# Optimization experiments

Hardware: AMD Instinct MI355X
Metric: run time of the kernel (lower is better)

Reference implementation:

```python
import jax, jax.numpy as jnp
import numpy as np


def _ln(x, g, b, eps=1e-5):
    mu = jnp.mean(x, axis=-1, keepdims=True)
    var = jnp.mean((x - mu) ** 2, axis=-1, keepdims=True)
    return (x - mu) / jnp.sqrt(var + eps) * g + b


def _cell(x, h, c, Wih, Whh, bih, bhh):
    # torch LSTM gate order: i, f, g, o
    gates = x @ Wih.T + h @ Whh.T + bih + bhh
    i, f, g, o = jnp.split(gates, 4, axis=-1)
    c_new = jax.nn.sigmoid(f) * c + jax.nn.sigmoid(i) * jnp.tanh(g)
    h_new = jax.nn.sigmoid(o) * jnp.tanh(c_new)
    return h_new, c_new


def _forward(physical, target_seq, enc_W1, enc_b1, enc_ln1_g, enc_ln1_b, enc_W2, enc_b2,
             enc_ln2_g, enc_ln2_b, Wih0, Whh0, bih0, bhh0, Wih1, Whh1, bih1, bhh1,
             ln_g, ln_b, proj_W, proj_b, head_W1, head_b1, head_W2, head_b2, init_input):
    B, T = target_seq.shape
    Hd = proj_b.shape[0]
    # physical encoder -> initial hidden (dropout in eval mode)
    e = jax.nn.relu(_ln(physical @ enc_W1.T + enc_b1, enc_ln1_g, enc_ln1_b))
    h0 = jnp.tanh(_ln(e @ enc_W2.T + enc_b2, enc_ln2_g, enc_ln2_b))  # (B,H)
    h_init = jnp.broadcast_to(h0, (2, 2, B, Hd))  # (layer, direction, B, H)
    c_init = jnp.zeros((2, 2, B, Hd), dtype=h0.dtype)
    # teacher forcing ratio = 1.0 -> inputs are known ahead of time
    x0 = jnp.broadcast_to(init_input, (B, 1))
    xs = jnp.concatenate([x0[None], jnp.swapaxes(target_seq, 0, 1)[:-1, :, None]], axis=0)  # (T,B,1)

    def step(carry, inp):
        h, c, prev = carry
        x, t = inp
        h0f, c0f = _cell(x, h[0, 0], c[0, 0], Wih0[0], Whh0[0], bih0[0], bhh0[0])
        h0b, c0b = _cell(x, h[0, 1], c[0, 1], Wih0[1], Whh0[1], bih0[1], bhh0[1])
        o0 = jnp.concatenate([h0f, h0b], axis=-1)  # (B,2H)
        h1f, c1f = _cell(o0, h[1, 0], c[1, 0], Wih1[0], Whh1[0], bih1[0], bhh1[0])
        h1b, c1b = _cell(o0, h[1, 1], c[1, 1], Wih1[1], Whh1[1], bih1[1], bhh1[1])
        out = _ln(jnp.concatenate([h1f, h1b], axis=-1), ln_g, ln_b)  # (B,2H)
        proj = out @ proj_W.T + proj_b  # (B,H)
        pred = jax.nn.relu(proj @ head_W1.T + head_b1) @ head_W2.T + head_b2  # (B,1)
        pred = jnp.where(t > 0, 0.8 * pred + 0.2 * prev, pred)
        h_new = jnp.stack([jnp.stack([h0f, h0b]), jnp.stack([h1f, h1b])])
        c_new = jnp.stack([jnp.stack([c0f, c0b]), jnp.stack([c1f, c1b])])
        return (h_new, c_new, pred), pred[:, 0]

    _, preds = jax.lax.scan(step, (h_init, c_init, jnp.zeros((B, 1), h0.dtype)),
                            (xs, jnp.arange(T)))
    return jnp.swapaxes(preds, 0, 1)  # (B,T)


def setup_inputs():
    B, P, Hd, T = 512, 16, 128, 128
    ks = iter(jax.random.split(jax.random.key(0), 40))
    rn = lambda shape, s=0.05: jax.random.normal(next(ks), shape, dtype=jnp.float32) * s
    return {
        "physical": jax.random.normal(next(ks), (B, P), dtype=jnp.float32),
        "target_seq": jax.random.normal(next(ks), (B, T), dtype=jnp.float32),
        "enc_W1": rn((2 * Hd, P)), "enc_b1": jnp.zeros((2 * Hd,), jnp.float32),
        "enc_ln1_g": jnp.ones((2 * Hd,), jnp.float32), "enc_ln1_b": jnp.zeros((2 * Hd,), jnp.float32),
        "enc_W2": rn((Hd, 2 * Hd)), "enc_b2": jnp.zeros((Hd,), jnp.float32),
        "enc_ln2_g": jnp.ones((Hd,), jnp.float32), "enc_ln2_b": jnp.zeros((Hd,), jnp.float32),
        "Wih0": rn((2, 4 * Hd, 1)), "Whh0": rn((2, 4 * Hd, Hd)),
        "bih0": jnp.zeros((2, 4 * Hd), jnp.float32), "bhh0": jnp.zeros((2, 4 * Hd), jnp.float32),
        "Wih1": rn((2, 4 * Hd, 2 * Hd)), "Whh1": rn((2, 4 * Hd, Hd)),
        "bih1": jnp.zeros((2, 4 * Hd), jnp.float32), "bhh1": jnp.zeros((2, 4 * Hd), jnp.float32),
        "ln_g": jnp.ones((2 * Hd,), jnp.float32), "ln_b": jnp.zeros((2 * Hd,), jnp.float32),
        "proj_W": rn((Hd, 2 * Hd)), "proj_b": jnp.zeros((Hd,), jnp.float32),
        "head_W1": rn((Hd, Hd)), "head_b1": jnp.zeros((Hd,), jnp.float32),
        "head_W2": rn((1, Hd)), "head_b2": jnp.zeros((1,), jnp.float32),
        "init_input": rn((1,), 0.02),
    }


def reference(physical, target_seq, enc_W1, enc_b1, enc_ln1_g, enc_ln1_b, enc_W2, enc_b2,
              enc_ln2_g, enc_ln2_b, Wih0, Whh0, bih0, bhh0, Wih1, Whh1, bih1, bhh1,
              ln_g, ln_b, proj_W, proj_b, head_W1, head_b1, head_W2, head_b2, init_input):
    return _forward(physical, target_seq, enc_W1, enc_b1, enc_ln1_g, enc_ln1_b, enc_W2, enc_b2,
                    enc_ln2_g, enc_ln2_b, Wih0, Whh0, bih0, bhh0, Wih1, Whh1, bih1, bhh1,
                    ln_g, ln_b, proj_W, proj_b, head_W1, head_b1, head_W2, head_b2, init_input)
```

## Files before the change

kernel.cpp:

```cpp
#include <hip/hip_runtime.h>
#include <hip/hip_bf16.h>

#define BB 512
#define TT 128

typedef unsigned short u16;
typedef short v8s __attribute__((ext_vector_type(8)));
typedef float f32x4 __attribute__((ext_vector_type(4)));

#define L2E  1.4426950408889634f
#define L2E2 2.8853900817779268f

__device__ __forceinline__ u16 f2bf(float x){
  union { float f; unsigned int u; } v; v.f = x;
  unsigned int r = (v.u + 0x7fffu + ((v.u >> 16) & 1u)) >> 16;
  return (u16)r;
}
__device__ __forceinline__ float bf2f(u16 u){
  union { unsigned int i; float f; } v; v.i = ((unsigned int)u) << 16; return v.f;
}
__device__ __forceinline__ float lo_bits(unsigned u){
  union { unsigned int i; float f; } v; v.i = u << 16; return v.f;
}
__device__ __forceinline__ float hi_bits(unsigned u){
  union { unsigned int i; float f; } v; v.i = u & 0xffff0000u; return v.f;
}
__device__ __forceinline__ uint2 pack4(f32x4 a){
  uint2 r;
  asm("v_cvt_pk_bf16_f32 %0, %1, %2" : "=v"(r.x) : "v"(a[0]), "v"(a[1]));
  asm("v_cvt_pk_bf16_f32 %0, %1, %2" : "=v"(r.y) : "v"(a[2]), "v"(a[3]));
  return r;
}
__device__ __forceinline__ float rcp_f(float x){ return __builtin_amdgcn_rcpf(x); }
#if defined(__has_builtin)
#if __has_builtin(__builtin_amdgcn_exp2f)
#define EXP2(x) __builtin_amdgcn_exp2f(x)
#endif
#endif
#ifndef EXP2
__device__ __forceinline__ float __exp2_asm(float x){
  float r; asm("v_exp_f32 %0, %1" : "=v"(r) : "v"(x)); return r;
}
#define EXP2(x) __exp2_asm(x)
#endif
__device__ __forceinline__ float sigm2(float y){ return rcp_f(1.f + EXP2(-y)); }
__device__ __forceinline__ float tanh2(float y){ return fmaf(2.f, sigm2(y), -1.f); }

__device__ __forceinline__ float tanh_f(float x){
  float e = __expf(-2.f * fabsf(x));
  float r = (1.f - e) * rcp_f(1.f + e);
  return copysignf(r, x);
}
__device__ __forceinline__ void bar_lds(){
  __builtin_amdgcn_sched_barrier(0);
  asm volatile("s_waitcnt lgkmcnt(0)" ::: "memory");
  __builtin_amdgcn_s_barrier();
  __builtin_amdgcn_sched_barrier(0);
}

__global__ __launch_bounds__(256) void k_prep(
    const float* tseq, const float* init_in,
    const float* Wih0, const float* Whh0, const float* bih0, const float* bhh0,
    const float* Wih1, const float* Whh1, const float* bih1, const float* bhh1,
    const float* projW, const float* hW1,
    float* xs, u16* W0p, u16* W1ip, u16* W1hp, u16* projWp, u16* hW1p,
    float* bias0, float* bias1, float* wv0)
{
  int tid = blockIdx.x * blockDim.x + threadIdx.x;
  int stride = gridDim.x * blockDim.x;
  for (int i = tid; i < TT*BB; i += stride){
    int t = i / BB, b = i % BB;
    xs[i] = (t == 0) ? init_in[0] : tseq[b*TT + (t-1)];
  }
  for (int i = tid; i < 2*512*128; i += stride){
    int d = i / (512*128), r = i % (512*128);
    int j = r / 128, k = r % 128;
    float sc = ((j >> 7) == 2) ? L2E2 : L2E;
    int dst = ((((d*32 + (j>>4))*4 + (k>>5))*64) + ((j&15) + 16*((k&31)>>3)))*8 + (k&7);
    W0p[dst]  = f2bf(Whh0[i] * sc);
    W1hp[dst] = f2bf(Whh1[i] * sc);
  }
  for (int i = tid; i < 2*512*256; i += stride){
    int d = i / (512*256), r = i % (512*256);
    int j = r / 256, k = r % 256;
    float sc = ((j >> 7) == 2) ? L2E2 : L2E;
    int dst = ((((d*32 + (j>>4))*8 + (k>>5))*64) + ((j&15) + 16*((k&31)>>3)))*8 + (k&7);
    W1ip[dst] = f2bf(Wih1[i] * sc);
  }
  for (int i = tid; i < 128*256; i += stride){
    int j = i / 256, k = i % 256;
    int dst = ((((j>>4)*8 + (k>>5))*64) + ((j&15) + 16*((k&31)>>3)))*8 + (k&7);
    projWp[dst] = f2bf(projW[i]);
  }
  for (int i = tid; i < 128*128; i += stride){
    int j = i / 128, k = i % 128;
    int dst = ((((j>>4)*4 + (k>>5))*64) + ((j&15) + 16*((k&31)>>3)))*8 + (k&7);
    hW1p[dst] = f2bf(hW1[i]);
  }
  for (int i = tid; i < 2*512; i += stride){
    float sc = (((i & 511) >> 7) == 2) ? L2E2 : L2E;
    bias0[i] = (bih0[i] + bhh0[i]) * sc;
    bias1[i] = (bih1[i] + bhh1[i]) * sc;
    wv0[i]   = Wih0[i] * sc;
  }
}

__global__ __launch_bounds__(256) void k_enc(
    const float* phys, const float* W1, const float* b1, const float* g1, const float* be1,
    const float* W2, const float* b2, const float* g2, const float* be2, float* h0enc)
{
  __shared__ float eL[8][256];
  int tid = threadIdx.x;
  int rr = tid >> 5, sub = tid & 31;
  int r = blockIdx.x * 8 + rr;
  float x[16];
#pragma unroll
  for (int k = 0; k < 16; ++k) x[k] = phys[r*16 + k];
  float y[8];
#pragma unroll
  for (int jj = 0; jj < 8; ++jj){
    int j = sub*8 + jj;
    float s = b1[j];
#pragma unroll
    for (int k = 0; k < 16; ++k) s += x[k] * W1[j*16 + k];
    y[jj] = s;
  }
  float sum = 0.f, sq = 0.f;
#pragma unroll
  for (int jj = 0; jj < 8; ++jj){ sum += y[jj]; sq += y[jj]*y[jj]; }
#pragma unroll
  for (int m = 16; m >= 1; m >>= 1){ sum += __shfl_xor(sum, m, 32); sq += __shfl_xor(sq, m, 32); }
  float mu = sum / 256.f;
  float rs = rsqrtf(sq / 256.f - mu*mu + 1e-5f);
#pragma unroll
  for (int jj = 0; jj < 8; ++jj){
    int j = sub*8 + jj;
    eL[rr][j] = fmaxf((y[jj] - mu) * rs * g1[j] + be1[j], 0.f);
  }
  __syncthreads();
  float y2[4];
#pragma unroll
  for (int jj = 0; jj < 4; ++jj){
    int j2 = sub*4 + jj;
    float s = b2[j2];
    const float* wrow = W2 + j2*256;
    for (int k = 0; k < 256; k += 4)
      s += eL[rr][k]*wrow[k] + eL[rr][k+1]*wrow[k+1] + eL[rr][k+2]*wrow[k+2] + eL[rr][k+3]*wrow[k+3];
    y2[jj] = s;
  }
  sum = 0.f; sq = 0.f;
#pragma unroll
  for (int jj = 0; jj < 4; ++jj){ sum += y2[jj]; sq += y2[jj]*y2[jj]; }
#pragma unroll
  for (int m = 16; m >= 1; m >>= 1){ sum += __shfl_xor(sum, m, 32); sq += __shfl_xor(sq, m, 32); }
  mu = sum / 128.f;
  rs = rsqrtf(sq / 128.f - mu*mu + 1e-5f);
#pragma unroll
  for (int jj = 0; jj < 4; ++jj){
    int j2 = sub*4 + jj;
    h0enc[r*128 + j2] = tanh_f((y2[jj]-mu)*rs*g2[j2] + be2[j2]);
  }
}

__global__ __launch_bounds__(512) void k_l0(
    const u16* W0p, const float* bias0, const float* wv0, const float* xs,
    const float* h0enc, u16* o0pack)
{
  __shared__ __align__(16) u16 Xb[2][4][512];
  __shared__ __align__(16) float xl[TT*16];
  int bx = blockIdx.x;
  int tile = bx & 31, d = bx >> 5;
  int tid = threadIdx.x, w = tid >> 6, l = tid & 63;
  int r0 = tile * 16, lrow = l & 15, lk = l >> 4;

  for (int i = tid; i < TT*16; i += 512){
    int t = i >> 4, r = i & 15;
    xl[i] = xs[t*BB + r0 + r];
  }
  if (tid < 256){
    int kf = tid >> 6, ll = tid & 63;
    const float* src = h0enc + (r0 + (ll & 15))*128 + kf*32 + 8*(ll >> 4);
    u16* dstp = &Xb[0][kf][ll*8];
#pragma unroll
    for (int i = 0; i < 8; ++i) dstp[i] = f2bf(src[i]);
  }

  const u16* Wb = W0p + (size_t)d*32*4*512;
  v8s wa[4][4];
#pragma unroll
  for (int q = 0; q < 4; ++q)
#pragma unroll
    for (int kf = 0; kf < 4; ++kf)
      wa[q][kf] = *(const v8s*)(Wb + (size_t)(((w + 8*q)*4 + kf)*64 + l)*8);

  float bias[4][4], wv[4][4];
#pragma unroll
  for (int q = 0; q < 4; ++q){
    int tq = w + 8*q;
#pragma unroll
    for (int jj = 0; jj < 4; ++jj){
      int j = tq*16 + 4*lk + jj;
      bias[q][jj] = bias0[d*512 + j];
      wv[q][jj]   = wv0[d*512 + j];
    }
  }
  float c[4] = {0.f,0.f,0.f,0.f};
  int jout = w*16 + 4*lk;
  int kfx = jout >> 5;
  int sl  = lrow + 16*((jout & 31) >> 3);
  int eb  = jout & 7;
  int kfo = 4*d + kfx;
  __syncthreads();

#pragma unroll 2
  for (int t = 0; t < TT; ++t){
    int cur = t & 1, nxt = cur ^ 1;
    v8s bfr[4];
#pragma unroll
    for (int kf = 0; kf < 4; ++kf) bfr[kf] = *(const v8s*)&Xb[cur][kf][l*8];
    float xv = xl[t*16 + lrow];
    f32x4 acc[4];
#pragma unroll
    for (int q = 0; q < 4; ++q)
#pragma unroll
      for (int jj = 0; jj < 4; ++jj)
        acc[q][jj] = fmaf(xv, wv[q][jj], bias[q][jj]);
#pragma unroll
    for (int kf = 0; kf < 4; ++kf)
#pragma unroll
      for (int q = 0; q < 4; ++q)
        acc[q] = __builtin_amdgcn_mfma_f32_16x16x32_bf16(wa[q][kf], bfr[kf], acc[q], 0, 0, 0);
    f32x4 hv;
#pragma unroll
    for (int jj = 0; jj < 4; ++jj){
      float si = sigm2(acc[0][jj]);
      float sf = sigm2(acc[1][jj]);
      float tg = tanh2(acc[2][jj]);
      float so = sigm2(acc[3][jj]);
      float cn = fmaf(sf, c[jj], si*tg);
      c[jj] = cn;
      float s2 = sigm2(L2E2 * cn);
      hv[jj] = so * fmaf(2.f, s2, -1.f);
    }
    uint2 hp = pack4(hv);
    *(uint2*)&Xb[nxt][kfx][sl*8 + eb] = hp;
    size_t off = ((((size_t)t*32 + tile)*8 + kfo)*64 + sl)*8 + eb;
    *(uint2*)&o0pack[off] = hp;
    bar_lds();
  }
}

__global__ __launch_bounds__(256) void k_zgemm(
    const u16* W1ip, const float* bias1p, const u16* o0pack, u16* z1p)
{
  int bx = blockIdx.x;
  int nc = bx & 3, bg = (bx >> 2) & 7, t = bx >> 5;
  int w = threadIdx.x >> 6, l = threadIdx.x & 63;
  int btile = bg*4 + w;
  int lk4 = (l >> 4) * 4;
  v8s bfrag[8];
#pragma unroll
  for (int kf = 0; kf < 8; ++kf)
    bfrag[kf] = *(const v8s*)&o0pack[((((size_t)t*32 + btile)*8 + kf)*64 + l)*8];
  f32x4 acc[16];
#pragma unroll
  for (int nt = 0; nt < 16; ++nt){
    int ntg = nc*16 + nt;
    acc[nt] = *(const f32x4*)&bias1p[(ntg >> 5)*512 + (ntg & 31)*16 + lk4];
  }
#pragma unroll
  for (int kf = 0; kf < 8; ++kf){
#pragma unroll
    for (int nt = 0; nt < 16; ++nt){
      int ntg = nc*16 + nt;
      int dir = ntg >> 5, tl = ntg & 31;
      v8s a = *(const v8s*)&W1ip[((((size_t)dir*32 + tl)*8 + kf)*64 + l)*8];
      acc[nt] = __builtin_amdgcn_mfma_f32_16x16x32_bf16(a, bfrag[kf], acc[nt], 0, 0, 0);
    }
  }
#pragma unroll
  for (int nt = 0; nt < 16; ++nt){
    int ntg = nc*16 + nt;
    uint2 zp = pack4(acc[nt]);
    *(uint2*)&z1p[((((size_t)t*32 + btile)*64 + ntg)*64 + l)*4] = zp;
  }
}

__global__ __launch_bounds__(512) void k_l1(
    const u16* W1hp, const u16* z1p, const float* h0enc, u16* h1b)
{
  __shared__ __align__(16) u16 Xh[2][4][512];
  int bx = blockIdx.x;
  int tile = bx & 31, d = bx >> 5;
  int tid = threadIdx.x, w = tid >> 6, l = tid & 63;
  int r0 = tile * 16, lrow = l & 15, lk = l >> 4;

  if (tid < 256){
    int kf = tid >> 6, ll = tid & 63;
    const float* src = h0enc + (r0 + (ll & 15))*128 + kf*32 + 8*(ll >> 4);
    u16* dstp = &Xh[0][kf][ll*8];
#pragma unroll
    for (int i = 0; i < 8; ++i) dstp[i] = f2bf(src[i]);
  }

  const u16* Wh = W1hp + (size_t)d*32*4*512;
  v8s wh[4][4];
#pragma unroll
  for (int q = 0; q < 4; ++q)
#pragma unroll
    for (int kf = 0; kf < 4; ++kf)
      wh[q][kf] = *(const v8s*)(Wh + (size_t)(((w + 8*q)*4 + kf)*64 + l)*8);

  float c[4] = {0.f,0.f,0.f,0.f};
  int jout = w*16 + 4*lk;
  int kfx = jout >> 5;
  int sl  = lrow + 16*((jout & 31) >> 3);
  int eb  = jout & 7;
  int zcol = d*32 + w;

  uint2 zr[4], zn[4];
#pragma unroll
  for (int q = 0; q < 4; ++q)
    zr[q] = *(const uint2*)&z1p[(((size_t)tile*64 + zcol + 8*q)*64 + l)*4];
#pragma unroll
  for (int q = 0; q < 4; ++q)
    zn[q] = *(const uint2*)&z1p[((((size_t)1*32 + tile)*64 + zcol + 8*q)*64 + l)*4];
  __syncthreads();

#pragma unroll 2
  for (int t = 0; t < TT; ++t){
    int cur = t & 1, nxt = cur ^ 1;
    v8s bh[4];
#pragma unroll
    for (int kf = 0; kf < 4; ++kf) bh[kf] = *(const v8s*)&Xh[cur][kf][l*8];
    f32x4 acc[4];
#pragma unroll
    for (int q = 0; q < 4; ++q){
      acc[q][0] = lo_bits(zr[q].x);
      acc[q][1] = hi_bits(zr[q].x);
      acc[q][2] = lo_bits(zr[q].y);
      acc[q][3] = hi_bits(zr[q].y);
    }
#pragma unroll
    for (int kf = 0; kf < 4; ++kf)
#pragma unroll
      for (int q = 0; q < 4; ++q)
        acc[q] = __builtin_amdgcn_mfma_f32_16x16x32_bf16(wh[q][kf], bh[kf], acc[q], 0, 0, 0);
    f32x4 hv;
#pragma unroll
    for (int jj = 0; jj < 4; ++jj){
      float si = sigm2(acc[0][jj]);
      float sf = sigm2(acc[1][jj]);
      float tg = tanh2(acc[2][jj]);
      float so = sigm2(acc[3][jj]);
      float cn = fmaf(sf, c[jj], si*tg);
      c[jj] = cn;
      float s2 = sigm2(L2E2 * cn);
      hv[jj] = so * fmaf(2.f, s2, -1.f);
    }
    uint2 hp = pack4(hv);
    *(uint2*)&Xh[nxt][kfx][sl*8 + eb] = hp;
    int hidx = ((t*BB + r0 + lrow) << 8) + (d << 7) + jout;
    *(uint2*)&h1b[hidx] = hp;
#pragma unroll
    for (int q = 0; q < 4; ++q) zr[q] = zn[q];
    int tp = (t + 2 < TT) ? t + 2 : TT - 1;
#pragma unroll
    for (int q = 0; q < 4; ++q)
      zn[q] = *(const uint2*)&z1p[((((size_t)tp*32 + tile)*64 + zcol + 8*q)*64 + l)*4];
    bar_lds();
  }
}

__global__ __launch_bounds__(256) void k_head(
    const u16* h1b, const float* lng, const float* lnb,
    const u16* projWp, const float* projb,
    const u16* hW1p, const float* hb1, const float* hW2, const float* hb2,
    float* qout)
{
  __shared__ __align__(16) u16 xls[4][16*256];
  __shared__ __align__(16) u16 pls[4][16*128];
  int w = threadIdx.x >> 6, l = threadIdx.x & 63;
  size_t g0 = (size_t)blockIdx.x*64 + w*16;
  int row = l >> 2, qc = l & 3;

  const u16* srcb = h1b + (g0 + row)*256;
  f32x4 v[16];
#pragma unroll
  for (int m = 0; m < 16; ++m){
    uint2 p = *(const uint2*)&srcb[m*16 + qc*4];
    v[m][0] = lo_bits(p.x);
    v[m][1] = hi_bits(p.x);
    v[m][2] = lo_bits(p.y);
    v[m][3] = hi_bits(p.y);
  }
  float sum = 0.f, sq = 0.f;
#pragma unroll
  for (int m = 0; m < 16; ++m){
#pragma unroll
    for (int i = 0; i < 4; ++i){ sum += v[m][i]; sq += v[m][i]*v[m][i]; }
  }
  sum += __shfl_xor(sum, 1); sq += __shfl_xor(sq, 1);
  sum += __shfl_xor(sum, 2); sq += __shfl_xor(sq, 2);
  float mu = sum / 256.f;
  float rs = rsqrtf(sq / 256.f - mu*mu + 1e-5f);
  u16* xw = xls[w];
  int rsw = (row & 7) << 3;
#pragma unroll
  for (int m = 0; m < 16; ++m){
    int cb = m*16 + qc*4;
    f32x4 gq = *(const f32x4*)&lng[cb];
    f32x4 bq = *(const f32x4*)&lnb[cb];
    f32x4 xn;
#pragma unroll
    for (int i = 0; i < 4; ++i) xn[i] = (v[m][i]-mu)*rs*gq[i] + bq[i];
    *(uint2*)&xw[(row*256 + cb) ^ rsw] = pack4(xn);
  }

  int lk = l >> 4, r = l & 15;
  int rsw2 = (r & 7) << 3;
  f32x4 acc[8];
#pragma unroll
  for (int nt = 0; nt < 8; ++nt) acc[nt] = *(const f32x4*)&projb[nt*16 + lk*4];
#pragma unroll
  for (int kf = 0; kf < 8; ++kf){
    v8s b = *(const v8s*)&xw[(r*256 + kf*32 + lk*8) ^ rsw2];
#pragma unroll
    for (int nt = 0; nt < 8; ++nt){
      v8s a = *(const v8s*)&projWp[(((size_t)nt*8 + kf)*64 + l)*8];
      acc[nt] = __builtin_amdgcn_mfma_f32_16x16x32_bf16(a, b, acc[nt], 0, 0, 0);
    }
  }
  u16* pw = pls[w];
#pragma unroll
  for (int nt = 0; nt < 8; ++nt)
    *(uint2*)&pw[(r*128 + nt*16 + lk*4) ^ rsw2] = pack4(acc[nt]);

  f32x4 acc2[8];
#pragma unroll
  for (int nt = 0; nt < 8; ++nt) acc2[nt] = *(const f32x4*)&hb1[nt*16 + lk*4];
#pragma unroll
  for (int kf = 0; kf < 4; ++kf){
    v8s b = *(const v8s*)&pw[(r*128 + kf*32 + lk*8) ^ rsw2];
#pragma unroll
    for (int nt = 0; nt < 8; ++nt){
      v8s a = *(const v8s*)&hW1p[(((size_t)nt*4 + kf)*64 + l)*8];
      acc2[nt] = __builtin_amdgcn_mfma_f32_16x16x32_bf16(a, b, acc2[nt], 0, 0, 0);
    }
  }
  float part = 0.f;
#pragma unroll
  for (int nt = 0; nt < 8; ++nt){
    f32x4 w2 = *(const f32x4*)&hW2[nt*16 + lk*4];
#pragma unroll
    for (int jj = 0; jj < 4; ++jj) part += fmaxf(acc2[nt][jj], 0.f) * w2[jj];
  }
  part += __shfl_xor(part, 16);
  part += __shfl_xor(part, 32);
  if (l < 16) qout[g0 + l] = part + hb2[0];
}

__global__ __launch_bounds__(512) void k_blend(const float* qout, float* out)
{
  int b = threadIdx.x;
  float pred = 0.f;
  for (int t0 = 0; t0 < TT; t0 += 16){
    float v[16];
#pragma unroll
    for (int i = 0; i < 16; ++i) v[i] = qout[(t0+i)*BB + b];
#pragma unroll
    for (int i = 0; i < 16; ++i){
      pred = (t0 + i == 0) ? v[i] : 0.8f*v[i] + 0.2f*pred;
      out[b*TT + t0 + i] = pred;
    }
  }
}

extern "C" void kernel_launch(void* const* d_in, const int* in_sizes, int n_in,
                              void* d_out, int out_size, void* d_ws, size_t ws_size,
                              hipStream_t stream) {
  const float* physical   = (const float*)d_in[0];
  const float* target_seq = (const float*)d_in[1];
  const float* enc_W1     = (const float*)d_in[2];
  const float* enc_b1     = (const float*)d_in[3];
  const float* enc_ln1_g  = (const float*)d_in[4];
  const float* enc_ln1_b  = (const float*)d_in[5];
  const float* enc_W2     = (const float*)d_in[6];
  const float* enc_b2     = (const float*)d_in[7];
  const float* enc_ln2_g  = (const float*)d_in[8];
  const float* enc_ln2_b  = (const float*)d_in[9];
  const float* Wih0       = (const float*)d_in[10];
  const float* Whh0       = (const float*)d_in[11];
  const float* bih0       = (const float*)d_in[12];
  const float* bhh0       = (const float*)d_in[13];
  const float* Wih1       = (const float*)d_in[14];
  const float* Whh1       = (const float*)d_in[15];
  const float* bih1       = (const float*)d_in[16];
  const float* bhh1       = (const float*)d_in[17];
  const float* ln_g       = (const float*)d_in[18];
  const float* ln_b       = (const float*)d_in[19];
  const float* proj_W     = (const float*)d_in[20];
  const float* proj_b     = (const float*)d_in[21];
  const float* head_W1    = (const float*)d_in[22];
  const float* head_b1    = (const float*)d_in[23];
  const float* head_W2    = (const float*)d_in[24];
  const float* head_b2    = (const float*)d_in[25];
  const float* init_input = (const float*)d_in[26];

  size_t off = 0;
  char* base = (char*)d_ws;
  auto carve = [&](size_t bytes) -> void* {
    void* p = base + off;
    off += (bytes + 255) & ~(size_t)255;
    return p;
  };
  u16*   o0pack  = (u16*)  carve((size_t)TT*32*8*64*8*2);
  u16*   h1b     = (u16*)  carve((size_t)TT*BB*256*2);
  u16*   z1p     = (u16*)  carve((size_t)TT*32*64*64*4*2);
  float* qout    = (float*)carve((size_t)TT*BB*4);
  float* h0enc   = (float*)carve((size_t)BB*128*4);
  float* xs      = (float*)carve((size_t)TT*BB*4);
  u16*   W0p     = (u16*)  carve((size_t)2*512*128*2);
  u16*   W1ip    = (u16*)  carve((size_t)2*512*256*2);
  u16*   W1hp    = (u16*)  carve((size_t)2*512*128*2);
  u16*   projWp  = (u16*)  carve((size_t)128*256*2);
  u16*   hW1p    = (u16*)  carve((size_t)128*128*2);
  float* bias0   = (float*)carve(4096);
  float* bias1   = (float*)carve(4096);
  float* wv0     = (float*)carve(4096);

  k_prep<<<256, 256, 0, stream>>>(target_seq, init_input, Wih0, Whh0, bih0, bhh0,
                                  Wih1, Whh1, bih1, bhh1, proj_W, head_W1,
                                  xs, W0p, W1ip, W1hp, projWp, hW1p,
                                  bias0, bias1, wv0);
  k_enc<<<64, 256, 0, stream>>>(physical, enc_W1, enc_b1, enc_ln1_g, enc_ln1_b,
                                enc_W2, enc_b2, enc_ln2_g, enc_ln2_b, h0enc);
  k_l0<<<64, 512, 0, stream>>>(W0p, bias0, wv0, xs, h0enc, o0pack);
  k_zgemm<<<4096, 256, 0, stream>>>(W1ip, bias1, o0pack, z1p);
  k_l1<<<64, 512, 0, stream>>>(W1hp, z1p, h0enc, h1b);
  k_head<<<1024, 256, 0, stream>>>(h1b, ln_g, ln_b, projWp, proj_b,
                                   hW1p, head_b1, head_W2, head_b2, qout);
  k_blend<<<1, 512, 0, stream>>>(qout, (float*)d_out);
}
```

Before: 376.7 us.

## Stage layer-1 input weights in LDS and split zgemm into more blocks

The layer-1 input-projection GEMM kernel now loads its weight fragments once per block into shared memory in two K-phases. All four waves then reuse them from LDS instead of each wave reading them from global memory. The N dimension per block is halved (8 tiles instead of 16), and the grid doubles to 8192 blocks, which cuts accumulator registers. The trade-off is extra barriers, 32KB of LDS per block, and twice as many reloads of the activation fragments. Unused helpers and the exp2 builtin fallback are also removed.

```diff
diff --git a/kernel.cpp b/kernel.cpp
--- a/kernel.cpp
+++ b/kernel.cpp
@@ -15,9 +15,6 @@
   union { float f; unsigned int u; } v; v.f = x;
   unsigned int r = (v.u + 0x7fffu + ((v.u >> 16) & 1u)) >> 16;
   return (u16)r;
-}
-__device__ __forceinline__ float bf2f(u16 u){
-  union { unsigned int i; float f; } v; v.i = ((unsigned int)u) << 16; return v.f;
 }
 __device__ __forceinline__ float lo_bits(unsigned u){
   union { unsigned int i; float f; } v; v.i = u << 16; return v.f;
@@ -32,18 +29,10 @@
   return r;
 }
 __device__ __forceinline__ float rcp_f(float x){ return __builtin_amdgcn_rcpf(x); }
-#if defined(__has_builtin)
-#if __has_builtin(__builtin_amdgcn_exp2f)
-#define EXP2(x) __builtin_amdgcn_exp2f(x)
-#endif
-#endif
-#ifndef EXP2
-__device__ __forceinline__ float __exp2_asm(float x){
+__device__ __forceinline__ float exp2_f(float x){
   float r; asm("v_exp_f32 %0, %1" : "=v"(r) : "v"(x)); return r;
 }
-#define EXP2(x) __exp2_asm(x)
-#endif
-__device__ __forceinline__ float sigm2(float y){ return rcp_f(1.f + EXP2(-y)); }
+__device__ __forceinline__ float sigm2(float y){ return rcp_f(1.f + exp2_f(-y)); }
 __device__ __forceinline__ float tanh2(float y){ return fmaf(2.f, sigm2(y), -1.f); }
 
 __device__ __forceinline__ float tanh_f(float x){
@@ -253,34 +242,50 @@
 __global__ __launch_bounds__(256) void k_zgemm(
     const u16* W1ip, const float* bias1p, const u16* o0pack, u16* z1p)
 {
+  __shared__ __align__(16) u16 Wl[8][4][64][8];
   int bx = blockIdx.x;
-  int nc = bx & 3, bg = (bx >> 2) & 7, t = bx >> 5;
-  int w = threadIdx.x >> 6, l = threadIdx.x & 63;
+  int nc = bx & 7, bg = (bx >> 3) & 7, t = bx >> 6;
+  int tid = threadIdx.x;
+  int w = tid >> 6, l = tid & 63;
   int btile = bg*4 + w;
   int lk4 = (l >> 4) * 4;
+  const u16* Wsrc = W1ip + (size_t)nc*8*8*64*8;
+  u16* WlF = &Wl[0][0][0][0];
+
   v8s bfrag[8];
 #pragma unroll
   for (int kf = 0; kf < 8; ++kf)
     bfrag[kf] = *(const v8s*)&o0pack[((((size_t)t*32 + btile)*8 + kf)*64 + l)*8];
-  f32x4 acc[16];
-#pragma unroll
-  for (int nt = 0; nt < 16; ++nt){
-    int ntg = nc*16 + nt;
+  f32x4 acc[8];
+#pragma unroll
+  for (int nt = 0; nt < 8; ++nt){
+    int ntg = nc*8 + nt;
     acc[nt] = *(const f32x4*)&bias1p[(ntg >> 5)*512 + (ntg & 31)*16 + lk4];
   }
 #pragma unroll
-  for (int kf = 0; kf < 8; ++kf){
-#pragma unroll
-    for (int nt = 0; nt < 16; ++nt){
-      int ntg = nc*16 + nt;
-      int dir = ntg >> 5, tl = ntg & 31;
-      v8s a = *(const v8s*)&W1ip[((((size_t)dir*32 + tl)*8 + kf)*64 + l)*8];
-      acc[nt] = __builtin_amdgcn_mfma_f32_16x16x32_bf16(a, bfrag[kf], acc[nt], 0, 0, 0);
-    }
-  }
-#pragma unroll
-  for (int nt = 0; nt < 16; ++nt){
-    int ntg = nc*16 + nt;
+  for (int ph = 0; ph < 2; ++ph){
+    if (ph) __syncthreads();
+#pragma unroll
+    for (int i = 0; i < 8; ++i){
+      int cid = i*256 + tid;
+      int nt = cid >> 8, r = cid & 255;
+      v8s v = *(const v8s*)&Wsrc[(size_t)(nt*8 + ph*4)*512 + r*8];
+      *(v8s*)&WlF[cid*8] = v;
+    }
+    __syncthreads();
+#pragma unroll
+    for (int kq = 0; kq < 4; ++kq){
+      int kf = ph*4 + kq;
+#pragma unroll
+      for (int nt = 0; nt < 8; ++nt){
+        v8s a = *(const v8s*)&Wl[nt][kq][l][0];
+        acc[nt] = __builtin_amdgcn_mfma_f32_16x16x32_bf16(a, bfrag[kf], acc[nt], 0, 0, 0);
+      }
+    }
+  }
+#pragma unroll
+  for (int nt = 0; nt < 8; ++nt){
+    int ntg = nc*8 + nt;
     uint2 zp = pack4(acc[nt]);
     *(uint2*)&z1p[((((size_t)t*32 + btile)*64 + ntg)*64 + l)*4] = zp;
   }
@@ -536,7 +541,7 @@
   k_enc<<<64, 256, 0, stream>>>(physical, enc_W1, enc_b1, enc_ln1_g, enc_ln1_b,
                                 enc_W2, enc_b2, enc_ln2_g, enc_ln2_b, h0enc);
   k_l0<<<64, 512, 0, stream>>>(W0p, bias0, wv0, xs, h0enc, o0pack);
-  k_zgemm<<<4096, 256, 0, stream>>>(W1ip, bias1, o0pack, z1p);
+  k_zgemm<<<8192, 256, 0, stream>>>(W1ip, bias1, o0pack, z1p);
   k_l1<<<64, 512, 0, stream>>>(W1hp, z1p, h0enc, h1b);
   k_head<<<1024, 256, 0, stream>>>(h1b, ln_g, ln_b, projWp, proj_b,
                                    hW1p, head_b1, head_W2, head_b2, qout);
```

Result: faster. 368.1 us (-2.3%).
